# Optimization experiments

Hardware: AMD Instinct MI355X
Metric: run time of the kernel (lower is better)

## Reference

```python
import jax, jax.numpy as jnp
import numpy as np

N_ENT = 100000
N_REL = 500
D = 200  # rank[0]==rank[1]==rank[2]
B = 512


def setup_inputs() -> dict:
    key = jax.random.key(0)
    k1, k2, k3, k4, k5, k6 = jax.random.split(key, 6)
    X_subj = jax.random.randint(k5, (B,), 0, N_ENT)
    X_rel = jax.random.randint(k6, (B,), 0, N_REL)
    X = jnp.stack([X_subj, X_rel], axis=1)  # [B, 2] int
    return {
        "X": X,
        "E1": jax.random.normal(k1, (N_ENT, D), dtype=jnp.float32) * 0.1,
        "R": jax.random.normal(k2, (N_REL, D), dtype=jnp.float32) * 0.1,
        "E2": jax.random.normal(k3, (N_ENT, D), dtype=jnp.float32) * 0.1,
        "W": jax.random.normal(k4, (D, D, D), dtype=jnp.float32) * 0.05,
    }


def reference(X, E1, R, E2, W):
    # sparse one-hot @ dense == direct gather (row select)
    e1 = E1[X[:, 0]]                 # [B, D]
    r = R[X[:, 1]]                   # [B, D]
    # torch: W.view(r.size(1), -1) reshapes (D,D,D) row-major -> (D, D*D),
    # so relation contracts over W's FIRST axis.
    W_mat = jnp.einsum('bi,ijk->bjk', r, W)    # [B, D, D]
    x = jnp.einsum('bj,bjk->bk', e1, W_mat)    # [B, D]
    logits = x @ E2.T                           # [B, N_ENT]
    return jax.nn.sigmoid(logits)
```

## Files before the change

### kernel.cpp

```cpp
#include <hip/hip_runtime.h>
#include <cstdint>
#include <cstddef>

#define DDIM 200
#define KPAD 224
#define BATCH 512
#define NENT 100000
#define KFLAT 40000
#define SPLIT 50
#define CHUNK_K 800
#define K1_BM 64
#define E1P 216
#define BROW 232

typedef __attribute__((ext_vector_type(8))) short bf16x8;
typedef __attribute__((ext_vector_type(4))) float f32x4;
typedef __attribute__((ext_vector_type(4))) unsigned short u16x4;
typedef unsigned short u16;

__device__ inline u16 f2bf(float f) {
    union { float f; uint32_t u; } v; v.f = f;
    uint32_t u = v.u;
    u += 0x7FFFu + ((u >> 16) & 1u);
    return (u16)(u >> 16);
}
__device__ inline float bf2f(u16 b) {
    union { uint32_t u; float f; } v; v.u = ((uint32_t)b) << 16;
    return v.f;
}

__global__ __launch_bounds__(256) void transpose_w_bf16(
    const float* __restrict__ W, u16* __restrict__ Wt)
{
    __shared__ u16 T[DDIM][72];
    const int tid = threadIdx.x;
    const int ij0 = blockIdx.x * 64;

    for (int l = tid; l < 64 * 50; l += 256) {
        int m = l & 63, c4 = l >> 6;
        f32x4 v = *(const f32x4*)&W[(size_t)(ij0 + m) * DDIM + c4 * 4];
        #pragma unroll
        for (int q = 0; q < 4; ++q) T[c4 * 4 + q][m] = f2bf(v[q]);
    }
    __syncthreads();
    for (int l = tid; l < DDIM * 8; l += 256) {
        int n = l >> 3, g = l & 7;
        *(bf16x8*)&Wt[(size_t)n * KFLAT + ij0 + g * 8] =
            *(const bf16x8*)&T[n][g * 8];
    }
}

__global__ __launch_bounds__(256) void tucker_x_partial(
    const int* __restrict__ X, const float* __restrict__ E1,
    const float* __restrict__ R, const u16* __restrict__ Wt,
    float* __restrict__ x_part)
{
    __shared__ u16   e1_s[K1_BM][E1P];
    __shared__ float r_s[K1_BM][4];
    __shared__ u16   At[K1_BM][40];
    __shared__ u16   Bt[208][40];

    const int tid = threadIdx.x;
    const int b0 = blockIdx.x * K1_BM;
    const int chunk = blockIdx.y;
    const int i0 = chunk * 4;
    const int kflat0 = chunk * CHUNK_K;

    for (int l = tid; l < K1_BM * 50; l += 256) {
        int m = l / 50, c4 = l - (l / 50) * 50;
        int subj = X[(b0 + m) * 2 + 0];
        f32x4 v = *(const f32x4*)&E1[(size_t)subj * DDIM + c4 * 4];
        u16x4 b;
        b[0] = f2bf(v[0]); b[1] = f2bf(v[1]); b[2] = f2bf(v[2]); b[3] = f2bf(v[3]);
        *(u16x4*)&e1_s[m][c4 * 4] = b;
    }
    if (tid < K1_BM * 4) {
        int m = tid >> 2, q = tid & 3;
        int rel = X[(b0 + m) * 2 + 1];
        r_s[m][q] = R[(size_t)rel * DDIM + i0 + q];
    }
    for (int l = tid; l < 8 * 40; l += 256)
        Bt[200 + l / 40][l % 40] = 0;

    const int wid = tid >> 6, lane = tid & 63;
    const int lr = lane & 15, lq = lane >> 4;

    f32x4 acc[13];
    #pragma unroll
    for (int f = 0; f < 13; ++f)
        #pragma unroll
        for (int q = 0; q < 4; ++q) acc[f][q] = 0.f;

    for (int s = 0; s < CHUNK_K / 32; ++s) {
        __syncthreads();
        {
            int m = tid >> 2, kb = (tid & 3) * 8;
            int base = s * 32 + kb;
            int io = base / DDIM;
            int j0 = base - io * DDIM;
            float rv = r_s[m][io];
            bf16x8 ev = *(const bf16x8*)&e1_s[m][j0];
            bf16x8 av;
            #pragma unroll
            for (int e = 0; e < 8; ++e)
                av[e] = (short)f2bf(rv * bf2f((u16)ev[e]));
            *(bf16x8*)&At[m][kb] = av;
        }
        for (int l = tid; l < DDIM * 4; l += 256) {
            int n = l >> 2, g = l & 3;
            *(bf16x8*)&Bt[n][g * 8] =
                *(const bf16x8*)&Wt[(size_t)n * KFLAT + kflat0 + s * 32 + g * 8];
        }
        __syncthreads();
        bf16x8 af = *(const bf16x8*)&At[wid * 16 + lr][lq * 8];
        #pragma unroll
        for (int f = 0; f < 13; ++f) {
            bf16x8 bfr = *(const bf16x8*)&Bt[f * 16 + lr][lq * 8];
            acc[f] = __builtin_amdgcn_mfma_f32_16x16x32_bf16(af, bfr, acc[f], 0, 0, 0);
        }
    }

    float* dst = x_part + ((size_t)chunk * BATCH + b0) * DDIM;
    #pragma unroll
    for (int f = 0; f < 13; ++f) {
        int n = f * 16 + lr;
        if (n < DDIM) {
            #pragma unroll
            for (int r4 = 0; r4 < 4; ++r4) {
                int m = wid * 16 + lq * 4 + r4;
                dst[(size_t)m * DDIM + n] = acc[f][r4];
            }
        }
    }
}

__global__ __launch_bounds__(256) void reduce_x(
    const float* __restrict__ part, u16* __restrict__ xbf)
{
    int id = blockIdx.x * 256 + threadIdx.x;
    if (id < BATCH * KPAD) {
        int b = id / KPAD, c = id - (id / KPAD) * KPAD;
        float s = 0.f;
        if (c < DDIM) {
            #pragma unroll 10
            for (int ch = 0; ch < SPLIT; ++ch)
                s += part[(size_t)ch * BATCH * DDIM + b * DDIM + c];
        }
        xbf[id] = f2bf(s);
    }
}

__global__ __launch_bounds__(512) void logits_sigmoid_mfma(
    const u16* __restrict__ xbf, const float* __restrict__ E2,
    float* __restrict__ out)
{
    __shared__ __align__(16) unsigned char lds_pool[8 * 16 * 72 * 4];
    u16   (*Bs)[BROW]   = (u16 (*)[BROW])lds_pool;
    float (*Ts)[16][72] = (float (*)[16][72])lds_pool;

    const int tid = threadIdx.x;
    const int n0 = blockIdx.x * 64;
    const int wid = tid >> 6, lane = tid & 63;
    const int lr = lane & 15, lq = lane >> 4;

    for (int l = tid; l < 64 * 50; l += 512) {
        int row = l / 50, c4 = l - (l / 50) * 50;
        int gn = n0 + row;
        u16x4 bb; bb[0] = 0; bb[1] = 0; bb[2] = 0; bb[3] = 0;
        if (gn < NENT) {
            f32x4 v = *(const f32x4*)&E2[(size_t)gn * DDIM + c4 * 4];
            bb[0] = f2bf(v[0]); bb[1] = f2bf(v[1]);
            bb[2] = f2bf(v[2]); bb[3] = f2bf(v[3]);
        }
        *(u16x4*)&Bs[row][c4 * 4] = bb;
    }
    {
        int row = tid >> 3, g = tid & 7;
        u16x4 z; z[0] = 0; z[1] = 0; z[2] = 0; z[3] = 0;
        *(u16x4*)&Bs[row][200 + g * 4] = z;
    }
    __syncthreads();

    f32x4 acc[4][4];
    #pragma unroll
    for (int fm = 0; fm < 4; ++fm)
        #pragma unroll
        for (int fn = 0; fn < 4; ++fn)
            #pragma unroll
            for (int q = 0; q < 4; ++q) acc[fm][fn][q] = 0.f;

    #pragma unroll
    for (int s = 0; s < 7; ++s) {
        bf16x8 af[4];
        #pragma unroll
        for (int fm = 0; fm < 4; ++fm) {
            int row = wid * 64 + fm * 16 + lr;
            af[fm] = *(const bf16x8*)&xbf[row * KPAD + s * 32 + lq * 8];
        }
        bf16x8 bfr[4];
        #pragma unroll
        for (int fn = 0; fn < 4; ++fn)
            bfr[fn] = *(const bf16x8*)&Bs[fn * 16 + lr][s * 32 + lq * 8];
        #pragma unroll
        for (int fm = 0; fm < 4; ++fm)
            #pragma unroll
            for (int fn = 0; fn < 4; ++fn)
                acc[fm][fn] = __builtin_amdgcn_mfma_f32_16x16x32_bf16(
                    af[fm], bfr[fn], acc[fm][fn], 0, 0, 0);
    }

    __syncthreads();

    #pragma unroll
    for (int fm = 0; fm < 4; ++fm) {
        int gm0 = wid * 64 + fm * 16;
        #pragma unroll
        for (int fn = 0; fn < 4; ++fn)
            #pragma unroll
            for (int r4 = 0; r4 < 4; ++r4)
                Ts[wid][lq * 4 + r4][fn * 16 + lr] = acc[fm][fn][r4];
        #pragma unroll
        for (int rr = 0; rr < 4; ++rr) {
            int row = rr * 4 + lq;
            f32x4 v = *(const f32x4*)&Ts[wid][row][lr * 4];
            f32x4 o;
            #pragma unroll
            for (int q = 0; q < 4; ++q)
                o[q] = __builtin_amdgcn_rcpf(1.0f + __expf(-v[q]));
            int gn = n0 + lr * 4;
            if (gn < NENT)
                __builtin_nontemporal_store(o,
                    (f32x4*)&out[(size_t)(gm0 + row) * NENT + gn]);
        }
    }
}

extern "C" void kernel_launch(void* const* d_in, const int* in_sizes, int n_in,
                              void* d_out, int out_size, void* d_ws, size_t ws_size,
                              hipStream_t stream) {
    const int*   X  = (const int*)d_in[0];
    const float* E1 = (const float*)d_in[1];
    const float* R  = (const float*)d_in[2];
    const float* E2 = (const float*)d_in[3];
    const float* W  = (const float*)d_in[4];
    float* out = (float*)d_out;

    float* x_part = (float*)d_ws;
    u16*   xbf    = (u16*)(x_part + (size_t)SPLIT * BATCH * DDIM);
    u16*   Wt     = xbf + (size_t)BATCH * KPAD;

    transpose_w_bf16<<<KFLAT / 64, 256, 0, stream>>>(W, Wt);
    tucker_x_partial<<<dim3(BATCH / K1_BM, SPLIT), 256, 0, stream>>>(
        X, E1, R, Wt, x_part);
    reduce_x<<<dim3((BATCH * KPAD + 255) / 256), 256, 0, stream>>>(x_part, xbf);
    logits_sigmoid_mfma<<<dim3((NENT + 63) / 64), 512, 0, stream>>>(xbf, E2, out);
}
```

Measured before the change: 144.9 us.

## Widen logits tile to 256 entities with 1024-thread blocks and row-staged epilogue

The logits kernel now tiles 256 entities per block with 16 waves arranged as 8 M-groups by 2 N-groups. Each wave keeps a 64x128 accumulator tile, which raises the MFMA work done per A-fragment load of xbf. The epilogue stages one 64-row slab at a time through shared memory, so each wave writes 256 contiguous floats per output row, giving longer coalesced stores of the 205 MB output. In exchange, register pressure roughly doubles (128 accumulator floats per lane) and the epilogue needs 16 barriers. It also launches only about 391 blocks, which could leave CUs underfilled or cause spills.

After: 378.1 us. 2.61x slower.

```diff
diff --git a/kernel.cpp b/kernel.cpp
--- a/kernel.cpp
+++ b/kernel.cpp
@@ -11,7 +11,8 @@
 #define CHUNK_K 800
 #define K1_BM 64
 #define E1P 216
-#define BROW 232
+#define K2_TN 256
+#define TS_W 268
 
 typedef __attribute__((ext_vector_type(8))) short bf16x8;
 typedef __attribute__((ext_vector_type(4))) float f32x4;
@@ -150,42 +151,43 @@
     }
 }
 
-__global__ __launch_bounds__(512) void logits_sigmoid_mfma(
+__global__ __launch_bounds__(1024) void logits_sigmoid_mfma(
     const u16* __restrict__ xbf, const float* __restrict__ E2,
     float* __restrict__ out)
 {
-    __shared__ __align__(16) unsigned char lds_pool[8 * 16 * 72 * 4];
-    u16   (*Bs)[BROW]   = (u16 (*)[BROW])lds_pool;
-    float (*Ts)[16][72] = (float (*)[16][72])lds_pool;
+    __shared__ __align__(16) unsigned char pool[K2_TN * 232 * 2];
+    u16   (*Bs)[232]  = (u16 (*)[232])pool;
+    float (*Ts)[TS_W] = (float (*)[TS_W])pool;
 
     const int tid = threadIdx.x;
-    const int n0 = blockIdx.x * 64;
+    const int n0 = blockIdx.x * K2_TN;
     const int wid = tid >> 6, lane = tid & 63;
+    const int mg = wid >> 1, ng = wid & 1;
     const int lr = lane & 15, lq = lane >> 4;
 
-    for (int l = tid; l < 64 * 50; l += 512) {
-        int row = l / 50, c4 = l - (l / 50) * 50;
+    for (int l = tid; l < K2_TN * 28; l += 1024) {
+        int row = l / 28, g = l - (l / 28) * 28;
         int gn = n0 + row;
-        u16x4 bb; bb[0] = 0; bb[1] = 0; bb[2] = 0; bb[3] = 0;
-        if (gn < NENT) {
-            f32x4 v = *(const f32x4*)&E2[(size_t)gn * DDIM + c4 * 4];
-            bb[0] = f2bf(v[0]); bb[1] = f2bf(v[1]);
-            bb[2] = f2bf(v[2]); bb[3] = f2bf(v[3]);
-        }
-        *(u16x4*)&Bs[row][c4 * 4] = bb;
-    }
-    {
-        int row = tid >> 3, g = tid & 7;
-        u16x4 z; z[0] = 0; z[1] = 0; z[2] = 0; z[3] = 0;
-        *(u16x4*)&Bs[row][200 + g * 4] = z;
+        u16x4 a4; a4[0] = 0; a4[1] = 0; a4[2] = 0; a4[3] = 0;
+        u16x4 b4; b4[0] = 0; b4[1] = 0; b4[2] = 0; b4[3] = 0;
+        if (g < 25 && gn < NENT) {
+            f32x4 v0 = *(const f32x4*)&E2[(size_t)gn * DDIM + g * 8];
+            f32x4 v1 = *(const f32x4*)&E2[(size_t)gn * DDIM + g * 8 + 4];
+            a4[0] = f2bf(v0[0]); a4[1] = f2bf(v0[1]);
+            a4[2] = f2bf(v0[2]); a4[3] = f2bf(v0[3]);
+            b4[0] = f2bf(v1[0]); b4[1] = f2bf(v1[1]);
+            b4[2] = f2bf(v1[2]); b4[3] = f2bf(v1[3]);
+        }
+        *(u16x4*)&Bs[row][g * 8]     = a4;
+        *(u16x4*)&Bs[row][g * 8 + 4] = b4;
     }
     __syncthreads();
 
-    f32x4 acc[4][4];
+    f32x4 acc[4][8];
     #pragma unroll
     for (int fm = 0; fm < 4; ++fm)
         #pragma unroll
-        for (int fn = 0; fn < 4; ++fn)
+        for (int fn = 0; fn < 8; ++fn)
             #pragma unroll
             for (int q = 0; q < 4; ++q) acc[fm][fn][q] = 0.f;
 
@@ -194,43 +196,47 @@
         bf16x8 af[4];
         #pragma unroll
         for (int fm = 0; fm < 4; ++fm) {
-            int row = wid * 64 + fm * 16 + lr;
+            int row = mg * 64 + fm * 16 + lr;
             af[fm] = *(const bf16x8*)&xbf[row * KPAD + s * 32 + lq * 8];
         }
-        bf16x8 bfr[4];
-        #pragma unroll
-        for (int fn = 0; fn < 4; ++fn)
-            bfr[fn] = *(const bf16x8*)&Bs[fn * 16 + lr][s * 32 + lq * 8];
+        bf16x8 bfr[8];
+        #pragma unroll
+        for (int fn = 0; fn < 8; ++fn)
+            bfr[fn] = *(const bf16x8*)&Bs[ng * 128 + fn * 16 + lr][s * 32 + lq * 8];
         #pragma unroll
         for (int fm = 0; fm < 4; ++fm)
             #pragma unroll
-            for (int fn = 0; fn < 4; ++fn)
+            for (int fn = 0; fn < 8; ++fn)
                 acc[fm][fn] = __builtin_amdgcn_mfma_f32_16x16x32_bf16(
                     af[fm], bfr[fn], acc[fm][fn], 0, 0, 0);
     }
 
-    __syncthreads();
-
-    #pragma unroll
-    for (int fm = 0; fm < 4; ++fm) {
-        int gm0 = wid * 64 + fm * 16;
-        #pragma unroll
-        for (int fn = 0; fn < 4; ++fn)
-            #pragma unroll
-            for (int r4 = 0; r4 < 4; ++r4)
-                Ts[wid][lq * 4 + r4][fn * 16 + lr] = acc[fm][fn][r4];
+    for (int c = 0; c < 8; ++c) {
+        __syncthreads();
+        if (mg == c) {
+            #pragma unroll
+            for (int fm = 0; fm < 4; ++fm)
+                #pragma unroll
+                for (int fn = 0; fn < 8; ++fn)
+                    #pragma unroll
+                    for (int r4 = 0; r4 < 4; ++r4)
+                        Ts[fm * 16 + lq * 4 + r4][ng * 128 + fn * 16 + lr] =
+                            acc[fm][fn][r4];
+        }
+        __syncthreads();
         #pragma unroll
         for (int rr = 0; rr < 4; ++rr) {
-            int row = rr * 4 + lq;
-            f32x4 v = *(const f32x4*)&Ts[wid][row][lr * 4];
+            int row = wid * 4 + rr;
+            f32x4 v = *(const f32x4*)&Ts[row][lane * 4];
             f32x4 o;
             #pragma unroll
-            for (int q = 0; q < 4; ++q)
-                o[q] = __builtin_amdgcn_rcpf(1.0f + __expf(-v[q]));
-            int gn = n0 + lr * 4;
+            for (int j = 0; j < 4; ++j)
+                o[j] = __builtin_amdgcn_rcpf(1.0f + __expf(-v[j]));
+            int gm = c * 64 + row;
+            int gn = n0 + lane * 4;
             if (gn < NENT)
                 __builtin_nontemporal_store(o,
-                    (f32x4*)&out[(size_t)(gm0 + row) * NENT + gn]);
+                    (f32x4*)&out[(size_t)gm * NENT + gn]);
         }
     }
 }
@@ -253,5 +259,6 @@
     tucker_x_partial<<<dim3(BATCH / K1_BM, SPLIT), 256, 0, stream>>>(
         X, E1, R, Wt, x_part);
     reduce_x<<<dim3((BATCH * KPAD + 255) / 256), 256, 0, stream>>>(x_part, xbf);
-    logits_sigmoid_mfma<<<dim3((NENT + 63) / 64), 512, 0, stream>>>(xbf, E2, out);
-}
+    logits_sigmoid_mfma<<<(NENT + K2_TN - 1) / K2_TN, 1024, 0, stream>>>(
+        xbf, E2, out);
+}
```
